# Kernel tuning notes

Measured on AMD Instinct MI355X. Metric: run time of the kernel, lower is better.

The kernel has to match this reference:

```python
import jax, jax.numpy as jnp
import numpy as np

B, N, D, NH, MAXLEN = 2, 2048, 1024, 16, 2048
HD = D // NH

def srel_skew(x):
    # x: [B, H, n, n] -> music-transformer skew
    b, h, n, _ = x.shape
    v = jnp.pad(x, ((0, 0), (0, 0), (0, 0), (1, 0)))  # pad last dim left
    return v.reshape(b, h, n + 1, n)[:, :, :n, :]

def split_head(x):
    # [B, n, D] -> [B, H, n, HD]
    b, n, _ = x.shape
    return x.reshape(b, n, NH, HD).transpose(0, 2, 1, 3)

def setup_inputs() -> dict:
    key = jax.random.key(0)
    ks = jax.random.split(key, 7)
    scale = 0.02
    return {
        "x": jax.random.normal(ks[0], (B, N, D), dtype=jnp.float32),
        "Wq": jax.random.normal(ks[1], (D, D), dtype=jnp.float32) * scale,
        "Wk": jax.random.normal(ks[2], (D, D), dtype=jnp.float32) * scale,
        "Wv": jax.random.normal(ks[3], (D, D), dtype=jnp.float32) * scale,
        "Wp": jax.random.normal(ks[4], (D, D), dtype=jnp.float32) * scale,
        "bp": jnp.zeros((D,), dtype=jnp.float32),
        "rel_embed": jax.random.normal(ks[5], (MAXLEN, D), dtype=jnp.float32) * scale,
    }

def reference(x, Wq, Wk, Wv, Wp, bp, rel_embed):
    b, n, d = x.shape
    qx = split_head(x @ Wq.T)  # [B,H,n,HD]
    kx = split_head(x @ Wk.T)
    vx = split_head(x @ Wv.T)
    # relative distance embeddings for last n positions
    ns = jnp.arange(n) + (MAXLEN - n)
    ex = rel_embed[ns].reshape(n, NH, HD).transpose(1, 0, 2)  # [H,n,HD]
    srel = srel_skew(jnp.einsum('bhnd,hmd->bhnm', qx, ex))  # [B,H,n,n]
    inv_dim = 1.0 / np.sqrt(d / NH)
    qk = (jnp.einsum('bhnd,bhmd->bhnm', qx, kx) + srel) * inv_dim
    mask = 1e9 * jnp.triu(jnp.ones((n, n), dtype=x.dtype), 1)
    atten = jax.nn.softmax(qk - mask, axis=-1)
    out = jnp.einsum('bhnm,bhmd->bhnd', atten, vx).transpose(0, 2, 1, 3).reshape(b, n, d)
    return out @ Wp.T + bp
```

## Files before the change

### kernel.cpp

```cpp
#include <hip/hip_runtime.h>

typedef __attribute__((ext_vector_type(8))) short short8;
typedef __attribute__((ext_vector_type(4))) float f32x4;
typedef unsigned short u16t;
typedef unsigned int u32t;

#define MFMA16(a,b,c) __builtin_amdgcn_mfma_f32_16x16x32_bf16((a),(b),(c),0,0,0)

constexpr int Bc = 2, Nc = 2048, Dc = 1024, NHc = 16, HDc = 64;
constexpr int EStride = Nc + 80;

__device__ __forceinline__ u16t f2bf(float f) {
  union { float f; u32t u; } v; v.f = f;
  u32t r = v.u + 0x7FFFu + ((v.u >> 16) & 1u);
  return (u16t)(r >> 16);
}
__device__ __forceinline__ u16t f2bfr(float f) {
  union { float f; u32t u; } v; v.f = f;
  return (u16t)((v.u + 0x8000u) >> 16);
}
__device__ __forceinline__ float bf2f(u16t b) {
  union { u32t u; float f; } v; v.u = (u32t)b << 16;
  return v.f;
}

template<int CTRL>
__device__ __forceinline__ float dppf(float x) {
  int xi = __builtin_bit_cast(int, x);
  int r = __builtin_amdgcn_update_dpp(0, xi, CTRL, 0xF, 0xF, true);
  return __builtin_bit_cast(float, r);
}
__device__ __forceinline__ float rsum16(float v) {
  v += dppf<0xB1>(v);
  v += dppf<0x4E>(v);
  v += dppf<0x124>(v);
  v += dppf<0x128>(v);
  return v;
}

__device__ __forceinline__ void gld16(const u16t* g, u16t* l) {
  __builtin_amdgcn_global_load_lds(
      (const __attribute__((address_space(1))) unsigned int*)(g),
      (__attribute__((address_space(3))) unsigned int*)(l), 16, 0, 0);
}

__device__ __forceinline__ void cvt4(const float* s, u16t* d) {
  f32x4 v = *(const f32x4*)s;
  u32t p0 = (u32t)f2bf(v[0]) | ((u32t)f2bf(v[1]) << 16);
  u32t p1 = (u32t)f2bf(v[2]) | ((u32t)f2bf(v[3]) << 16);
  u32t* dp = (u32t*)d;
  dp[0] = p0; dp[1] = p1;
}

__global__ __launch_bounds__(256) void cvt_all(
    const float* __restrict__ x, const float* __restrict__ wq,
    const float* __restrict__ wk, const float* __restrict__ wv,
    const float* __restrict__ wp, const float* __restrict__ rel,
    u16t* __restrict__ xb, u16t* __restrict__ wqb, u16t* __restrict__ wkb,
    u16t* __restrict__ wvb, u16t* __restrict__ wpb, u16t* __restrict__ Eb) {
  int i = blockIdx.x * 256 + threadIdx.x;
  if (i < 1048576) {
    cvt4(x + (size_t)i * 4, xb + (size_t)i * 4);
  } else if (i < 2097152) {
    int r = i - 1048576;
    int w = r >> 18;
    int k = (r & 262143) * 4;
    const float* s = (w == 0) ? wq : (w == 1) ? wk : (w == 2) ? wv : wp;
    u16t* d = (w == 0) ? wqb : (w == 1) ? wkb : (w == 2) ? wvb : wpb;
    cvt4(s + k, d + k);
  } else if (i < 2621440) {
    int r = i - 2097152;
    int flat = r * 4;
    int h = flat >> 17;
    int rem = flat & 131071;
    int m = rem >> 6, d = rem & 63;
    cvt4(rel + (size_t)m * Dc + h * HDc + d,
         Eb + ((size_t)h * EStride + m) * HDc + d);
  } else {
    int r = i - 2621440;
    int flat = r * 4;
    int h = flat / 5120;
    int rem = flat - h * 5120;
    int pr = rem >> 6, d = rem & 63;
    u32t* dp = (u32t*)(Eb + ((size_t)h * EStride + Nc + pr) * HDc + d);
    dp[0] = 0; dp[1] = 0;
  }
}

__global__ __launch_bounds__(256, 3) void gemm_qkv(const u16t* __restrict__ A,
    const u16t* __restrict__ Wq, const u16t* __restrict__ Wk,
    const u16t* __restrict__ Wv, u16t* __restrict__ Qb,
    u16t* __restrict__ Kb, u16t* __restrict__ Vb) {
  __shared__ u16t lA[128 * 32];
  __shared__ u16t lB[128 * 32];
  const int y = blockIdx.y, which = y >> 3;
  const u16t* W = (which == 0) ? Wq : (which == 1) ? Wk : Wv;
  u16t* outb = (which == 0) ? Qb : (which == 1) ? Kb : Vb;
  const float sc = (which == 0) ? 0.18033688011112042f : 1.0f;
  const int m0 = blockIdx.x * 128, n0 = (y & 7) * 128;
  const int t = threadIdx.x, wave = t >> 6, lane = t & 63;
  const int l15 = lane & 15, q4 = lane >> 4, wm = wave & 1, wn = wave >> 1;
  const int srow = wave * 16 + (lane >> 2);
  const int scol = (lane & 3) * 8;

  f32x4 acc[4][4];
  for (int i = 0; i < 4; i++)
    for (int j = 0; j < 4; j++)
      for (int r = 0; r < 4; r++) acc[i][j][r] = 0.f;

  for (int k0 = 0; k0 < Dc; k0 += 32) {
    __syncthreads();
    for (int r = 0; r < 2; r++) {
      int row = srow + r * 64;
      gld16(A + (size_t)(m0 + row) * Dc + k0 + scol, lA + wave * 512 + r * 2048);
      gld16(W + (size_t)(n0 + row) * Dc + k0 + scol, lB + wave * 512 + r * 2048);
    }
    __syncthreads();
    short8 af[4], bf[4];
    for (int i = 0; i < 4; i++) {
      af[i] = *(const short8*)(&lA[(wm * 64 + i * 16 + l15) * 32 + q4 * 8]);
      bf[i] = *(const short8*)(&lB[(wn * 64 + i * 16 + l15) * 32 + q4 * 8]);
    }
    for (int mi = 0; mi < 4; mi++)
      for (int ni = 0; ni < 4; ni++)
        acc[mi][ni] = MFMA16(af[mi], bf[ni], acc[mi][ni]);
  }

  for (int mi = 0; mi < 4; mi++)
    for (int ni = 0; ni < 4; ni++)
      for (int rg = 0; rg < 4; rg++) {
        int gm = m0 + wm * 64 + mi * 16 + q4 * 4 + rg;
        int gn = n0 + wn * 64 + ni * 16 + l15;
        int b = gm >> 11, n = gm & 2047, h = gn >> 6, hd = gn & 63;
        outb[(((size_t)(b * NHc + h) * Nc + n) * HDc) + hd] =
            f2bf(acc[mi][ni][rg] * sc);
      }
}

__global__ __launch_bounds__(256, 2) void gemm_proj(const u16t* __restrict__ A,
    const u16t* __restrict__ W, float* __restrict__ outf,
    const float* __restrict__ bias) {
  __shared__ u16t lA[128 * 32];
  __shared__ u16t lB[128 * 32];
  const int m0 = blockIdx.x * 128, n0 = blockIdx.y * 128;
  const int t = threadIdx.x, wave = t >> 6, lane = t & 63;
  const int l15 = lane & 15, q4 = lane >> 4, wm = wave & 1, wn = wave >> 1;
  const int srow = wave * 16 + (lane >> 2);
  const int scol = (lane & 3) * 8;

  f32x4 acc[4][4];
  for (int i = 0; i < 4; i++)
    for (int j = 0; j < 4; j++)
      for (int r = 0; r < 4; r++) acc[i][j][r] = 0.f;

  for (int k0 = 0; k0 < Dc; k0 += 32) {
    __syncthreads();
    for (int r = 0; r < 2; r++) {
      int row = srow + r * 64;
      gld16(A + (size_t)(m0 + row) * Dc + k0 + scol, lA + wave * 512 + r * 2048);
      gld16(W + (size_t)(n0 + row) * Dc + k0 + scol, lB + wave * 512 + r * 2048);
    }
    __syncthreads();
    short8 af[4], bf[4];
    for (int i = 0; i < 4; i++) {
      af[i] = *(const short8*)(&lA[(wm * 64 + i * 16 + l15) * 32 + q4 * 8]);
      bf[i] = *(const short8*)(&lB[(wn * 64 + i * 16 + l15) * 32 + q4 * 8]);
    }
    for (int mi = 0; mi < 4; mi++)
      for (int ni = 0; ni < 4; ni++)
        acc[mi][ni] = MFMA16(af[mi], bf[ni], acc[mi][ni]);
  }

  for (int mi = 0; mi < 4; mi++)
    for (int ni = 0; ni < 4; ni++)
      for (int rg = 0; rg < 4; rg++) {
        int gm = m0 + wm * 64 + mi * 16 + q4 * 4 + rg;
        int gn = n0 + wn * 64 + ni * 16 + l15;
        outf[(size_t)gm * Dc + gn] = acc[mi][ni][rg] + bias[gn];
      }
}

__global__ __launch_bounds__(256) void transp_v(const u16t* __restrict__ Vb,
                                                u16t* __restrict__ Vt) {
  __shared__ u16t lt[64 * 72];
  int n0 = blockIdx.x * 64;
  int bh = blockIdx.y;
  const u16t* src = Vb + ((size_t)bh * Nc + n0) * HDc;
  u16t* dst = Vt + (size_t)bh * HDc * Nc + n0;
  int t = threadIdx.x;
  for (int c = t; c < 512; c += 256) {
    int r = c >> 3, c8 = c & 7;
    f32x4 raw = *(const f32x4*)(src + r * HDc + c8 * 8);
    const u16t* u = (const u16t*)&raw;
    for (int e = 0; e < 8; e++) lt[(c8 * 8 + e) * 72 + r] = u[e];
  }
  __syncthreads();
  for (int c = t; c < 512; c += 256) {
    int d = c >> 3, c8 = c & 7;
    *(f32x4*)(dst + (size_t)d * Nc + c8 * 8) = *(const f32x4*)(&lt[d * 72 + c8 * 8]);
  }
}

__global__ __launch_bounds__(256, 2) void attn(const u16t* __restrict__ Qb,
                                               const u16t* __restrict__ Kb,
                                               const u16t* __restrict__ Vt,
                                               const u16t* __restrict__ Eb,
                                               u16t* __restrict__ AO) {
  __shared__ u16t lK[64 * 72];
  __shared__ u16t lE[128 * 72];
  __shared__ u16t lV[64 * 72];
  __shared__ u16t lP[4][16 * 88];

  const int xbk = blockIdx.x;
  const int h = blockIdx.y, b = blockIdx.z;
  const u16t* Qh = Qb + (size_t)(b * NHc + h) * Nc * HDc;
  const u16t* Kh = Kb + (size_t)(b * NHc + h) * Nc * HDc;
  const u16t* Vh = Vt + (size_t)(b * NHc + h) * HDc * Nc;
  const u16t* Eh = Eb + (size_t)h * EStride * HDc;

  const int t = threadIdx.x, wave = t >> 6, lane = t & 63, l15 = lane & 15, q4 = lane >> 4;
  const int tbase = (3 - wave) * 16;
  u16t* Pw = lP[wave];

  const int sr = t >> 3, sc8 = (t & 7) * 8;
  const int sr2 = sr + 32;

  for (int ph = 0; ph < 2; ph++) {
    const int qi = ph ? xbk : (31 - xbk);
    const int r0 = qi * 64;
    const int rw = r0 + wave * 16;

    short8 qf[2], qsf[2];
    {
      int r = rw + l15;
      int rs = r - 1; if (rs < 0) rs = 0;
      for (int kh = 0; kh < 2; kh++) {
        qf[kh]  = *(const short8*)(Qh + (size_t)r * HDc + kh * 32 + q4 * 8);
        qsf[kh] = *(const short8*)(Qh + (size_t)rs * HDc + kh * 32 + q4 * 8);
      }
    }

    f32x4 accO[4];
    float l_p[4];
    for (int rg = 0; rg < 4; rg++) l_p[rg] = 0.f;
    for (int dt = 0; dt < 4; dt++)
      for (int rg = 0; rg < 4; rg++) accO[dt][rg] = 0.f;

    {
      *(f32x4*)(&lK[sr * 72 + sc8])  = *(const f32x4*)(Kh + (size_t)sr * HDc + sc8);
      *(f32x4*)(&lK[sr2 * 72 + sc8]) = *(const f32x4*)(Kh + (size_t)sr2 * HDc + sc8);
      *(f32x4*)(&lV[sr * 72 + sc8])  = *(const f32x4*)(Vh + (size_t)sr * Nc + sc8);
      *(f32x4*)(&lV[sr2 * 72 + sc8]) = *(const f32x4*)(Vh + (size_t)sr2 * Nc + sc8);
      const int ebase0 = Nc - 63 - r0;
      for (int i = 0; i < 4; i++) {
        int cc = t + i * 256;
        int s = cc >> 3, c8 = (cc & 7) * 8;
        *(f32x4*)(&lE[s * 72 + c8]) =
            *(const f32x4*)(Eh + (size_t)(ebase0 + s) * HDc + c8);
      }
    }

    for (int j = 0; j <= qi; j++) {
      const int c0 = j * 64;
      __syncthreads();

      f32x4 pK0, pK1, pV0, pV1, pE0, pE1;
      if (j < qi) {
        const int cn = c0 + 64;
        pK0 = *(const f32x4*)(Kh + (size_t)(cn + sr) * HDc + sc8);
        pK1 = *(const f32x4*)(Kh + (size_t)(cn + sr2) * HDc + sc8);
        pV0 = *(const f32x4*)(Vh + (size_t)sr * Nc + cn + sc8);
        pV1 = *(const f32x4*)(Vh + (size_t)sr2 * Nc + cn + sc8);
        const int ebn = 64 * (j + 1) - r0 + (Nc - 63) + 64;
        pE0 = *(const f32x4*)(Eh + (size_t)(ebn + sr) * HDc + sc8);
        pE1 = *(const f32x4*)(Eh + (size_t)(ebn + sr2) * HDc + sc8);
      }

      f32x4 accS[4];
      for (int ct = 0; ct < 4; ct++)
        for (int rg = 0; rg < 4; rg++) accS[ct][rg] = 0.f;
      for (int kh = 0; kh < 2; kh++)
        for (int ct = 0; ct < 4; ct++) {
          short8 bfr = *(const short8*)(&lK[(ct * 16 + l15) * 72 + kh * 32 + q4 * 8]);
          accS[ct] = MFMA16(qf[kh], bfr, accS[ct]);
        }
      const int rot = (j & 1) << 6;
      f32x4 accP[5];
      for (int pt = 0; pt < 5; pt++)
        for (int rg = 0; rg < 4; rg++) accP[pt][rg] = 0.f;
      for (int kh = 0; kh < 2; kh++)
        for (int pt = 0; pt < 5; pt++) {
          int prow = (tbase + pt * 16 + l15 + rot) & 127;
          short8 bfr = *(const short8*)(&lE[prow * 72 + kh * 32 + q4 * 8]);
          accP[pt] = MFMA16(qsf[kh], bfr, accP[pt]);
        }
      for (int pt = 0; pt < 5; pt++)
        for (int rg = 0; rg < 4; rg++)
          Pw[(q4 * 4 + rg) * 88 + pt * 16 + l15] = f2bfr(accP[pt][rg]);
      __asm__ volatile("s_waitcnt lgkmcnt(0)" ::: "memory");
      float pv[4][4];
      for (int ct = 0; ct < 4; ct++)
        for (int rg = 0; rg < 4; rg++) {
          int u16i = q4 * 4 + rg;
          float srel = bf2f(Pw[u16i * 88 + ct * 16 + 15 + l15 - u16i]);
          float s = accS[ct][rg] + srel;
          if (j == qi && (c0 + ct * 16 + l15) > (rw + u16i)) s = -1e30f;
          float p = exp2f(s);
          l_p[rg] += p;
          pv[ct][rg] = p;
        }
      __asm__ volatile("" ::: "memory");
      for (int ct = 0; ct < 4; ct++)
        for (int rg = 0; rg < 4; rg++)
          Pw[(q4 * 4 + rg) * 88 + ct * 16 + l15] = f2bfr(pv[ct][rg]);
      __asm__ volatile("s_waitcnt lgkmcnt(0)" ::: "memory");
      for (int kh = 0; kh < 2; kh++) {
        short8 af = *(const short8*)(&Pw[l15 * 88 + kh * 32 + q4 * 8]);
        for (int dt = 0; dt < 4; dt++) {
          short8 bfr = *(const short8*)(&lV[(dt * 16 + l15) * 72 + kh * 32 + q4 * 8]);
          accO[dt] = MFMA16(af, bfr, accO[dt]);
        }
      }

      __syncthreads();
      if (j < qi) {
        *(f32x4*)(&lK[sr * 72 + sc8])  = pK0;
        *(f32x4*)(&lK[sr2 * 72 + sc8]) = pK1;
        *(f32x4*)(&lV[sr * 72 + sc8])  = pV0;
        *(f32x4*)(&lV[sr2 * 72 + sc8]) = pV1;
        int ph0 = (sr + 64 * j) & 127;
        int ph1 = (sr2 + 64 * j) & 127;
        *(f32x4*)(&lE[ph0 * 72 + sc8]) = pE0;
        *(f32x4*)(&lE[ph1 * 72 + sc8]) = pE1;
      }
    }

    for (int rg = 0; rg < 4; rg++) {
      float inv = 1.f / rsum16(l_p[rg]);
      for (int dt = 0; dt < 4; dt++) {
        int r = rw + q4 * 4 + rg;
        int col = h * HDc + dt * 16 + l15;
        AO[((size_t)(b * Nc + r)) * Dc + col] = f2bf(accO[dt][rg] * inv);
      }
    }
  }
}

extern "C" void kernel_launch(void* const* d_in, const int* in_sizes, int n_in,
                              void* d_out, int out_size, void* d_ws, size_t ws_size,
                              hipStream_t stream) {
  (void)in_sizes; (void)n_in; (void)out_size; (void)ws_size;
  const float* x   = (const float*)d_in[0];
  const float* Wq  = (const float*)d_in[1];
  const float* Wk  = (const float*)d_in[2];
  const float* Wv  = (const float*)d_in[3];
  const float* Wp  = (const float*)d_in[4];
  const float* bp  = (const float*)d_in[5];
  const float* rel = (const float*)d_in[6];
  float* out = (float*)d_out;

  char* ws = (char*)d_ws;
  u16t* xb  = (u16t*)(ws);
  u16t* wqb = (u16t*)(ws + 8388608);
  u16t* wkb = (u16t*)(ws + 10485760);
  u16t* wvb = (u16t*)(ws + 12582912);
  u16t* wpb = (u16t*)(ws + 14680064);
  u16t* Eb  = (u16t*)(ws + 16777216);
  u16t* Qb  = (u16t*)(ws + 21233664);
  u16t* Kb  = (u16t*)(ws + 29622272);
  u16t* Vb  = (u16t*)(ws + 38010880);
  u16t* Vtb = (u16t*)(ws + 46399488);
  u16t* AOb = (u16t*)(ws + 54788096);

  cvt_all<<<10320, 256, 0, stream>>>(x, Wq, Wk, Wv, Wp, rel,
                                     xb, wqb, wkb, wvb, wpb, Eb);
  gemm_qkv<<<dim3(32, 24), 256, 0, stream>>>(xb, wqb, wkb, wvb, Qb, Kb, Vb);
  transp_v<<<dim3(32, 32), 256, 0, stream>>>(Vb, Vtb);
  attn<<<dim3(16, NHc, Bc), 256, 0, stream>>>(Qb, Kb, Vtb, Eb, AOb);
  gemm_proj<<<dim3(32, 8), 256, 0, stream>>>(AOb, wpb, out, bp);
}
```

Measured before the change: 231.2 us.

## Fuse V transpose into QKV GEMM and keep softmax probabilities in registers

The QKV GEMM epilogue now writes V directly in transposed layout, so the separate transpose kernel and its extra round trip through global memory go away. The attention kernel computes the transposed score tile (K·Q instead of Q·K). Its probability fragments can then feed a 16x16x16 bf16 MFMA for P·V straight from registers, with no LDS write and read-back. The relative-position scores are now staged as fp32 in LDS, and the output is written as packed 4-element stores. The trade-offs are more, smaller MFMAs for P·V, a larger fp32 LDS buffer, and strided V-transpose stores from the GEMM.

```diff
diff --git a/kernel.cpp b/kernel.cpp
--- a/kernel.cpp
+++ b/kernel.cpp
@@ -1,11 +1,21 @@
 #include <hip/hip_runtime.h>
 
 typedef __attribute__((ext_vector_type(8))) short short8;
+typedef __attribute__((ext_vector_type(4))) short s16x4;
 typedef __attribute__((ext_vector_type(4))) float f32x4;
 typedef unsigned short u16t;
 typedef unsigned int u32t;
 
 #define MFMA16(a,b,c) __builtin_amdgcn_mfma_f32_16x16x32_bf16((a),(b),(c),0,0,0)
+
+__device__ __forceinline__ f32x4 mfma16x16(s16x4 a, s16x4 b, f32x4 c) {
+#if __has_builtin(__builtin_amdgcn_mfma_f32_16x16x16bf16_1k)
+  return __builtin_amdgcn_mfma_f32_16x16x16bf16_1k(a, b, c, 0, 0, 0);
+#else
+  __asm__("v_mfma_f32_16x16x16_bf16 %0, %1, %2, %0" : "+v"(c) : "v"(a), "v"(b));
+  return c;
+#endif
+}
 
 constexpr int Bc = 2, Nc = 2048, Dc = 1024, NHc = 16, HDc = 64;
 constexpr int EStride = Nc + 80;
@@ -15,27 +25,15 @@
   u32t r = v.u + 0x7FFFu + ((v.u >> 16) & 1u);
   return (u16t)(r >> 16);
 }
-__device__ __forceinline__ u16t f2bfr(float f) {
-  union { float f; u32t u; } v; v.f = f;
-  return (u16t)((v.u + 0x8000u) >> 16);
-}
-__device__ __forceinline__ float bf2f(u16t b) {
-  union { u32t u; float f; } v; v.u = (u32t)b << 16;
-  return v.f;
-}
-
-template<int CTRL>
-__device__ __forceinline__ float dppf(float x) {
-  int xi = __builtin_bit_cast(int, x);
-  int r = __builtin_amdgcn_update_dpp(0, xi, CTRL, 0xF, 0xF, true);
-  return __builtin_bit_cast(float, r);
-}
-__device__ __forceinline__ float rsum16(float v) {
-  v += dppf<0xB1>(v);
-  v += dppf<0x4E>(v);
-  v += dppf<0x124>(v);
-  v += dppf<0x128>(v);
-  return v;
+__device__ __forceinline__ u32t pk2(float a, float b) {
+  u32t ua = __builtin_bit_cast(u32t, a);
+  u32t ub = __builtin_bit_cast(u32t, b);
+  return ((ua + 0x8000u) >> 16) | ((ub + 0x8000u) & 0xFFFF0000u);
+}
+__device__ __forceinline__ s16x4 pk4(float a, float b, float c, float d) {
+  union { u32t u[2]; s16x4 s; } r;
+  r.u[0] = pk2(a, b); r.u[1] = pk2(c, d);
+  return r.s;
 }
 
 __device__ __forceinline__ void gld16(const u16t* g, u16t* l) {
@@ -90,12 +88,11 @@
 __global__ __launch_bounds__(256, 3) void gemm_qkv(const u16t* __restrict__ A,
     const u16t* __restrict__ Wq, const u16t* __restrict__ Wk,
     const u16t* __restrict__ Wv, u16t* __restrict__ Qb,
-    u16t* __restrict__ Kb, u16t* __restrict__ Vb) {
+    u16t* __restrict__ Kb, u16t* __restrict__ Vt) {
   __shared__ u16t lA[128 * 32];
   __shared__ u16t lB[128 * 32];
   const int y = blockIdx.y, which = y >> 3;
   const u16t* W = (which == 0) ? Wq : (which == 1) ? Wk : Wv;
-  u16t* outb = (which == 0) ? Qb : (which == 1) ? Kb : Vb;
   const float sc = (which == 0) ? 0.18033688011112042f : 1.0f;
   const int m0 = blockIdx.x * 128, n0 = (y & 7) * 128;
   const int t = threadIdx.x, wave = t >> 6, lane = t & 63;
@@ -126,15 +123,29 @@
         acc[mi][ni] = MFMA16(af[mi], bf[ni], acc[mi][ni]);
   }
 
-  for (int mi = 0; mi < 4; mi++)
-    for (int ni = 0; ni < 4; ni++)
-      for (int rg = 0; rg < 4; rg++) {
-        int gm = m0 + wm * 64 + mi * 16 + q4 * 4 + rg;
+  if (which < 2) {
+    for (int mi = 0; mi < 4; mi++)
+      for (int ni = 0; ni < 4; ni++)
+        for (int rg = 0; rg < 4; rg++) {
+          int gm = m0 + wm * 64 + mi * 16 + q4 * 4 + rg;
+          int gn = n0 + wn * 64 + ni * 16 + l15;
+          int b = gm >> 11, n = gm & 2047, h = gn >> 6, hd = gn & 63;
+          u16t* outb = (which == 0) ? Qb : Kb;
+          outb[(((size_t)(b * NHc + h) * Nc + n) * HDc) + hd] =
+              f2bf(acc[mi][ni][rg] * sc);
+        }
+  } else {
+    for (int mi = 0; mi < 4; mi++)
+      for (int ni = 0; ni < 4; ni++) {
+        int gm = m0 + wm * 64 + mi * 16 + q4 * 4;
         int gn = n0 + wn * 64 + ni * 16 + l15;
         int b = gm >> 11, n = gm & 2047, h = gn >> 6, hd = gn & 63;
-        outb[(((size_t)(b * NHc + h) * Nc + n) * HDc) + hd] =
-            f2bf(acc[mi][ni][rg] * sc);
-      }
+        union { u32t u[2]; s16x4 s; } pkv;
+        pkv.u[0] = (u32t)f2bf(acc[mi][ni][0]) | ((u32t)f2bf(acc[mi][ni][1]) << 16);
+        pkv.u[1] = (u32t)f2bf(acc[mi][ni][2]) | ((u32t)f2bf(acc[mi][ni][3]) << 16);
+        *(s16x4*)(&Vt[((size_t)(b * NHc + h) * HDc + hd) * Nc + n]) = pkv.s;
+      }
+  }
 }
 
 __global__ __launch_bounds__(256, 2) void gemm_proj(const u16t* __restrict__ A,
@@ -180,27 +191,6 @@
       }
 }
 
-__global__ __launch_bounds__(256) void transp_v(const u16t* __restrict__ Vb,
-                                                u16t* __restrict__ Vt) {
-  __shared__ u16t lt[64 * 72];
-  int n0 = blockIdx.x * 64;
-  int bh = blockIdx.y;
-  const u16t* src = Vb + ((size_t)bh * Nc + n0) * HDc;
-  u16t* dst = Vt + (size_t)bh * HDc * Nc + n0;
-  int t = threadIdx.x;
-  for (int c = t; c < 512; c += 256) {
-    int r = c >> 3, c8 = c & 7;
-    f32x4 raw = *(const f32x4*)(src + r * HDc + c8 * 8);
-    const u16t* u = (const u16t*)&raw;
-    for (int e = 0; e < 8; e++) lt[(c8 * 8 + e) * 72 + r] = u[e];
-  }
-  __syncthreads();
-  for (int c = t; c < 512; c += 256) {
-    int d = c >> 3, c8 = c & 7;
-    *(f32x4*)(dst + (size_t)d * Nc + c8 * 8) = *(const f32x4*)(&lt[d * 72 + c8 * 8]);
-  }
-}
-
 __global__ __launch_bounds__(256, 2) void attn(const u16t* __restrict__ Qb,
                                                const u16t* __restrict__ Kb,
                                                const u16t* __restrict__ Vt,
@@ -209,7 +199,7 @@
   __shared__ u16t lK[64 * 72];
   __shared__ u16t lE[128 * 72];
   __shared__ u16t lV[64 * 72];
-  __shared__ u16t lP[4][16 * 88];
+  __shared__ float Ps[4][16 * 84];
 
   const int xbk = blockIdx.x;
   const int h = blockIdx.y, b = blockIdx.z;
@@ -220,7 +210,7 @@
 
   const int t = threadIdx.x, wave = t >> 6, lane = t & 63, l15 = lane & 15, q4 = lane >> 4;
   const int tbase = (3 - wave) * 16;
-  u16t* Pw = lP[wave];
+  float* Pw = Ps[wave];
 
   const int sr = t >> 3, sc8 = (t & 7) * 8;
   const int sr2 = sr + 32;
@@ -241,8 +231,7 @@
     }
 
     f32x4 accO[4];
-    float l_p[4];
-    for (int rg = 0; rg < 4; rg++) l_p[rg] = 0.f;
+    float l_p = 0.f;
     for (int dt = 0; dt < 4; dt++)
       for (int rg = 0; rg < 4; rg++) accO[dt][rg] = 0.f;
 
@@ -281,8 +270,8 @@
         for (int rg = 0; rg < 4; rg++) accS[ct][rg] = 0.f;
       for (int kh = 0; kh < 2; kh++)
         for (int ct = 0; ct < 4; ct++) {
-          short8 bfr = *(const short8*)(&lK[(ct * 16 + l15) * 72 + kh * 32 + q4 * 8]);
-          accS[ct] = MFMA16(qf[kh], bfr, accS[ct]);
+          short8 kfr = *(const short8*)(&lK[(ct * 16 + l15) * 72 + kh * 32 + q4 * 8]);
+          accS[ct] = MFMA16(kfr, qf[kh], accS[ct]);
         }
       const int rot = (j & 1) << 6;
       f32x4 accP[5];
@@ -291,36 +280,32 @@
       for (int kh = 0; kh < 2; kh++)
         for (int pt = 0; pt < 5; pt++) {
           int prow = (tbase + pt * 16 + l15 + rot) & 127;
-          short8 bfr = *(const short8*)(&lE[prow * 72 + kh * 32 + q4 * 8]);
-          accP[pt] = MFMA16(qsf[kh], bfr, accP[pt]);
+          short8 efr = *(const short8*)(&lE[prow * 72 + kh * 32 + q4 * 8]);
+          accP[pt] = MFMA16(efr, qsf[kh], accP[pt]);
         }
       for (int pt = 0; pt < 5; pt++)
-        for (int rg = 0; rg < 4; rg++)
-          Pw[(q4 * 4 + rg) * 88 + pt * 16 + l15] = f2bfr(accP[pt][rg]);
+        *(f32x4*)(&Pw[l15 * 84 + pt * 16 + q4 * 4]) = accP[pt];
       __asm__ volatile("s_waitcnt lgkmcnt(0)" ::: "memory");
+      const int rbase = l15 * 83 + q4 * 4 + 15;
       float pv[4][4];
       for (int ct = 0; ct < 4; ct++)
         for (int rg = 0; rg < 4; rg++) {
-          int u16i = q4 * 4 + rg;
-          float srel = bf2f(Pw[u16i * 88 + ct * 16 + 15 + l15 - u16i]);
+          float srel = Pw[rbase + ct * 16 + rg];
           float s = accS[ct][rg] + srel;
-          if (j == qi && (c0 + ct * 16 + l15) > (rw + u16i)) s = -1e30f;
+          if (j == qi && (c0 + ct * 16 + q4 * 4 + rg) > (rw + l15)) s = -1e30f;
           float p = exp2f(s);
-          l_p[rg] += p;
+          l_p += p;
           pv[ct][rg] = p;
         }
       __asm__ volatile("" ::: "memory");
-      for (int ct = 0; ct < 4; ct++)
-        for (int rg = 0; rg < 4; rg++)
-          Pw[(q4 * 4 + rg) * 88 + ct * 16 + l15] = f2bfr(pv[ct][rg]);
-      __asm__ volatile("s_waitcnt lgkmcnt(0)" ::: "memory");
-      for (int kh = 0; kh < 2; kh++) {
-        short8 af = *(const short8*)(&Pw[l15 * 88 + kh * 32 + q4 * 8]);
-        for (int dt = 0; dt < 4; dt++) {
-          short8 bfr = *(const short8*)(&lV[(dt * 16 + l15) * 72 + kh * 32 + q4 * 8]);
-          accO[dt] = MFMA16(af, bfr, accO[dt]);
-        }
-      }
+      s16x4 bq[4];
+      for (int ks = 0; ks < 4; ks++)
+        bq[ks] = pk4(pv[ks][0], pv[ks][1], pv[ks][2], pv[ks][3]);
+      for (int dt = 0; dt < 4; dt++)
+        for (int ks = 0; ks < 4; ks++) {
+          s16x4 vfr = *(const s16x4*)(&lV[(dt * 16 + l15) * 72 + ks * 16 + q4 * 4]);
+          accO[dt] = mfma16x16(vfr, bq[ks], accO[dt]);
+        }
 
       __syncthreads();
       if (j < qi) {
@@ -335,12 +320,16 @@
       }
     }
 
-    for (int rg = 0; rg < 4; rg++) {
-      float inv = 1.f / rsum16(l_p[rg]);
+    float l2 = l_p + __shfl_xor(l_p, 16);
+    float lt = l2 + __shfl_xor(l2, 32);
+    float inv = 1.f / lt;
+    {
+      int r = rw + l15;
+      u16t* dst = AO + (size_t)(b * Nc + r) * Dc + h * HDc + q4 * 4;
       for (int dt = 0; dt < 4; dt++) {
-        int r = rw + q4 * 4 + rg;
-        int col = h * HDc + dt * 16 + l15;
-        AO[((size_t)(b * Nc + r)) * Dc + col] = f2bf(accO[dt][rg] * inv);
+        s16x4 o = pk4(accO[dt][0] * inv, accO[dt][1] * inv,
+                      accO[dt][2] * inv, accO[dt][3] * inv);
+        *(s16x4*)(dst + dt * 16) = o;
       }
     }
   }
@@ -368,14 +357,12 @@
   u16t* Eb  = (u16t*)(ws + 16777216);
   u16t* Qb  = (u16t*)(ws + 21233664);
   u16t* Kb  = (u16t*)(ws + 29622272);
-  u16t* Vb  = (u16t*)(ws + 38010880);
-  u16t* Vtb = (u16t*)(ws + 46399488);
-  u16t* AOb = (u16t*)(ws + 54788096);
+  u16t* Vtb = (u16t*)(ws + 38010880);
+  u16t* AOb = (u16t*)(ws + 46399488);
 
   cvt_all<<<10320, 256, 0, stream>>>(x, Wq, Wk, Wv, Wp, rel,
                                      xb, wqb, wkb, wvb, wpb, Eb);
-  gemm_qkv<<<dim3(32, 24), 256, 0, stream>>>(xb, wqb, wkb, wvb, Qb, Kb, Vb);
-  transp_v<<<dim3(32, 32), 256, 0, stream>>>(Vb, Vtb);
+  gemm_qkv<<<dim3(32, 24), 256, 0, stream>>>(xb, wqb, wkb, wvb, Qb, Kb, Vtb);
   attn<<<dim3(16, NHc, Bc), 256, 0, stream>>>(Qb, Kb, Vtb, Eb, AOb);
   gemm_proj<<<dim3(32, 8), 256, 0, stream>>>(AOb, wpb, out, bp);
 }
```

Result: faster. 220.6 us (-4.6%).
